# Kernel tuning notes

Hardware: AMD Instinct MI355X
Metric: run time of the kernel (lower is better)

The kernel has to match this reference:

```python
import jax, jax.numpy as jnp
import numpy as np

HIDDEN = 4096
INTER = 11008
B, S = 8, 16
QMAX = 127  # int8 symmetric range for w_bits=8


def setup_inputs() -> dict:
    key = jax.random.key(0)
    ks = jax.random.split(key, 7)
    hidden_state = jax.random.normal(ks[0], (B, S, HIDDEN), dtype=jnp.float32)
    # Quantized weights stored as integer values in float32 (as the dequant source)
    w1_q = jax.random.randint(ks[1], (INTER, HIDDEN), -QMAX - 1, QMAX + 1).astype(jnp.float32)
    w3_q = jax.random.randint(ks[2], (INTER, HIDDEN), -QMAX - 1, QMAX + 1).astype(jnp.float32)
    w2_q = jax.random.randint(ks[3], (HIDDEN, INTER), -QMAX - 1, QMAX + 1).astype(jnp.float32)
    # Per-output-channel dequant scales (has_scale=True)
    w1_s = jax.random.uniform(ks[4], (INTER,), dtype=jnp.float32, minval=0.5, maxval=1.5) * 0.01
    w3_s = jax.random.uniform(ks[5], (INTER,), dtype=jnp.float32, minval=0.5, maxval=1.5) * 0.01
    w2_s = jax.random.uniform(ks[6], (HIDDEN,), dtype=jnp.float32, minval=0.5, maxval=1.5) * 0.01
    return {"hidden_state": hidden_state, "w1_q": w1_q, "w1_s": w1_s,
            "w3_q": w3_q, "w3_s": w3_s, "w2_q": w2_q, "w2_s": w2_s}


def _dequant_linear(x, w_q, w_s):
    # w_q: [out, in] integer-valued weights; w_s: [out] per-channel scale
    # y = x @ (w_q * w_s[:, None]).T == (x @ w_q.T) * w_s
    return jnp.einsum('bsh,oh->bso', x, w_q) * w_s


def reference(hidden_state, w1_q, w1_s, w3_q, w3_s, w2_q, w2_s):
    up = _dequant_linear(hidden_state, w1_q, w1_s)      # [B,S,INTER]
    gate = _dequant_linear(hidden_state, w3_q, w3_s)    # [B,S,INTER]
    h = jax.nn.silu(up) * gate                          # SwiGLU
    return _dequant_linear(h, w2_q, w2_s)               # [B,S,HIDDEN]
```

## Files before the change

kernel.cpp:

```cpp
#include <hip/hip_runtime.h>

#define HIDDEN 4096
#define INTER  11008
#define MTOK   128
#define NMERG  (2*INTER)
#define KS1    4
#define KS2    16

typedef short          short8  __attribute__((ext_vector_type(8)));
typedef unsigned short ushort8 __attribute__((ext_vector_type(8)));
typedef float          f32x16  __attribute__((ext_vector_type(16)));
#define AS1 __attribute__((address_space(1)))
#define AS3 __attribute__((address_space(3)))

static __device__ __forceinline__ unsigned short f2bf_rne(float f) {
    unsigned u = __builtin_bit_cast(unsigned, f);
    u += 0x7FFFu + ((u >> 16) & 1u);
    return (unsigned short)(u >> 16);
}
static __device__ __forceinline__ float bf2f(unsigned short b) {
    unsigned u = (unsigned)b << 16;
    return __builtin_bit_cast(float, u);
}
static __device__ __forceinline__ int pk2(float lo, float hi) {
    return (int)__builtin_amdgcn_perm(__builtin_bit_cast(unsigned, hi),
                                      __builtin_bit_cast(unsigned, lo),
                                      0x07060302u);
}

__global__ void cvt_x_k(const float* __restrict__ x, unsigned short* __restrict__ A2) {
    int f = blockIdx.x * 256 + threadIdx.x;
    int lane = f & 63, w = f >> 6;
    int kstep = w >> 2, ms = w & 3;
    int m = ms * 32 + (lane & 31);
    int k = kstep * 16 + (lane >> 5) * 8;
    const float* src = x + (size_t)m * HIDDEN + k;
    float4 v0 = *(const float4*)(src);
    float4 v1 = *(const float4*)(src + 4);
    ushort8 o;
    o[0] = f2bf_rne(v0.x); o[1] = f2bf_rne(v0.y); o[2] = f2bf_rne(v0.z); o[3] = f2bf_rne(v0.w);
    o[4] = f2bf_rne(v1.x); o[5] = f2bf_rne(v1.y); o[6] = f2bf_rne(v1.z); o[7] = f2bf_rne(v1.w);
    *(ushort8*)(A2 + (size_t)f * 8) = o;
}

template<bool OBF16>
__global__ __launch_bounds__(256) void gemm_k(
    const unsigned short* __restrict__ A2,
    const float* __restrict__ B0, const float* __restrict__ B1, int nhalf,
    void* __restrict__ part, int K, int N, int totTiles, int ksplit)
{
    __shared__ __align__(16) float lds[8192];
    const int lane = threadIdx.x & 63;
    const int ws   = threadIdx.x >> 6;
    const int n0   = blockIdx.x * 128;
    const int ks   = blockIdx.y;
    const int tbeg = (ks * totTiles) / ksplit;
    const int tend = ((ks + 1) * totTiles) / ksplit;

    const char* gbase[8];
#pragma unroll
    for (int i = 0; i < 8; ++i) {
        int s = ws * 512 + i * 64 + lane;
        int n = s >> 4;
        int a = (s & 15) ^ (n & 15);
        const float* rowp = (n0 + n < nhalf) ? (B0 + (size_t)(n0 + n) * K)
                                             : (B1 + (size_t)(n0 + n - nhalf) * K);
        gbase[i] = (const char*)rowp + a * 16;
    }

    f32x16 acc[4];
#pragma unroll
    for (int t = 0; t < 4; ++t)
#pragma unroll
        for (int r = 0; r < 16; ++r) acc[t][r] = 0.f;

    const int nl = ws * 32 + (lane & 31);

    for (int t = tbeg; t < tend; ++t) {
        const size_t koff = (size_t)t * 64 * 4;
#pragma unroll
        for (int i = 0; i < 8; ++i) {
            __builtin_amdgcn_global_load_lds(
                (const AS1 unsigned*)(gbase[i] + koff),
                (AS3 unsigned*)((char*)lds + ws * 8192 + i * 1024), 16, 0, 0);
        }
        __syncthreads();

#pragma unroll
        for (int step = 0; step < 4; ++step) {
            int a0 = step * 4 + ((lane >> 5) << 1);
            int p0 = nl * 16 + (a0 ^ (nl & 15));
            int p1 = nl * 16 + ((a0 + 1) ^ (nl & 15));
            float4 v0 = *(const float4*)((const char*)lds + p0 * 16);
            float4 v1 = *(const float4*)((const char*)lds + p1 * 16);
            int4 bi;
            bi.x = pk2(v0.x, v0.y); bi.y = pk2(v0.z, v0.w);
            bi.z = pk2(v1.x, v1.y); bi.w = pk2(v1.z, v1.w);
            short8 bf = __builtin_bit_cast(short8, bi);
            int kg = t * 4 + step;
#pragma unroll
            for (int ms = 0; ms < 4; ++ms) {
                short8 af = *(const short8*)(A2 + ((size_t)(kg * 4 + ms) * 64 + lane) * 8);
                acc[ms] = __builtin_amdgcn_mfma_f32_32x32x16_bf16(af, bf, acc[ms], 0, 0, 0);
            }
        }
        __syncthreads();
    }

    const int n = n0 + ws * 32 + (lane & 31);
#pragma unroll
    for (int ms = 0; ms < 4; ++ms)
#pragma unroll
        for (int r = 0; r < 16; ++r) {
            int m = ms * 32 + (r & 3) + 8 * (r >> 2) + 4 * (lane >> 5);
            size_t idx = ((size_t)ks * MTOK + m) * (size_t)N + n;
            if (OBF16) ((unsigned short*)part)[idx] = f2bf_rne(acc[ms][r]);
            else       ((float*)part)[idx] = acc[ms][r];
        }
}

__global__ void swiglu_k(const unsigned short* __restrict__ p1,
                         const float* __restrict__ s1, const float* __restrict__ s3,
                         unsigned short* __restrict__ h2)
{
    int f = blockIdx.x * 256 + threadIdx.x;
    int lane = f & 63, w = f >> 6;
    int kstep = w >> 2, ms = w & 3;
    int m = ms * 32 + (lane & 31);
    int j = kstep * 16 + (lane >> 5) * 8;
    float up[8], gt[8];
#pragma unroll
    for (int e = 0; e < 8; ++e) { up[e] = 0.f; gt[e] = 0.f; }
#pragma unroll
    for (int ks = 0; ks < KS1; ++ks) {
        const unsigned short* pu = p1 + ((size_t)ks * MTOK + m) * NMERG + j;
        ushort8 u = *(const ushort8*)(pu);
        ushort8 g = *(const ushort8*)(pu + INTER);
#pragma unroll
        for (int e = 0; e < 8; ++e) { up[e] += bf2f(u[e]); gt[e] += bf2f(g[e]); }
    }
    float4 c1a = *(const float4*)(s1 + j), c1b = *(const float4*)(s1 + j + 4);
    float4 c3a = *(const float4*)(s3 + j), c3b = *(const float4*)(s3 + j + 4);
    float c1[8] = {c1a.x, c1a.y, c1a.z, c1a.w, c1b.x, c1b.y, c1b.z, c1b.w};
    float c3[8] = {c3a.x, c3a.y, c3a.z, c3a.w, c3b.x, c3b.y, c3b.z, c3b.w};
    ushort8 o;
#pragma unroll
    for (int e = 0; e < 8; ++e) {
        float u = up[e] * c1[e], g = gt[e] * c3[e];
        o[e] = f2bf_rne(g * u / (1.f + __expf(-u)));
    }
    *(ushort8*)(h2 + (size_t)f * 8) = o;
}

__global__ void reduce_k(const float* __restrict__ p, const float* __restrict__ s2,
                         float* __restrict__ out)
{
    int i = (blockIdx.x * 256 + threadIdx.x) * 4;
    float4 acc = *(const float4*)(p + i);
#pragma unroll
    for (int s = 1; s < KS2; ++s) {
        float4 v = *(const float4*)(p + (size_t)s * MTOK * HIDDEN + i);
        acc.x += v.x; acc.y += v.y; acc.z += v.z; acc.w += v.w;
    }
    int ncol = i & (HIDDEN - 1);
    float4 sc = *(const float4*)(s2 + ncol);
    acc.x *= sc.x; acc.y *= sc.y; acc.z *= sc.z; acc.w *= sc.w;
    *(float4*)(out + i) = acc;
}

extern "C" void kernel_launch(void* const* d_in, const int* in_sizes, int n_in,
                              void* d_out, int out_size, void* d_ws, size_t ws_size,
                              hipStream_t stream) {
    const float* x   = (const float*)d_in[0];
    const float* w1q = (const float*)d_in[1];
    const float* w1s = (const float*)d_in[2];
    const float* w3q = (const float*)d_in[3];
    const float* w3s = (const float*)d_in[4];
    const float* w2q = (const float*)d_in[5];
    const float* w2s = (const float*)d_in[6];
    float* out = (float*)d_out;

    char* ws = (char*)d_ws;
    unsigned short* xb2 = (unsigned short*)ws;
    unsigned short* h2  = (unsigned short*)(ws + (1u << 20));
    void* part          = (void*)(ws + (4u << 20));

    cvt_x_k<<<MTOK * HIDDEN / 8 / 256, 256, 0, stream>>>(x, xb2);
    gemm_k<true><<<dim3(NMERG / 128, KS1), 256, 0, stream>>>(
        xb2, w1q, w3q, INTER, part, HIDDEN, NMERG, HIDDEN / 64, KS1);
    swiglu_k<<<MTOK * INTER / 8 / 256, 256, 0, stream>>>(
        (const unsigned short*)part, w1s, w3s, h2);
    gemm_k<false><<<dim3(HIDDEN / 128, KS2), 256, 0, stream>>>(
        h2, w2q, w2q, 1 << 30, part, INTER, HIDDEN, INTER / 64, KS2);
    reduce_k<<<MTOK * HIDDEN / 4 / 256, 256, 0, stream>>>(
        (const float*)part, w2s, out);
}
```

Before: 540.6 us.

## Restructure GEMM into independent per-wave 32-column tiles with larger K chunks

The GEMM kernel now gives each wave its own 32-column output tile and its own 32KB LDS buffer, with 128-thread blocks. Each wave streams a 256-wide K chunk per iteration using wave-level s_waitcnt instead of block-wide __syncthreads. The LDS swizzle becomes a lane-rotation scheme, and the second GEMM's split-K drops from 16 to 8, which also shrinks the partial-sum reduction. The aims are to remove block barriers and to put more weight bytes in flight per wave. The cost is 64KB of LDS per block, which limits occupancy, and no double buffering, so load latency is only hidden across waves.

Measured after the change: 781.4 us. +44.5%, slower.

```diff
diff --git a/kernel.cpp b/kernel.cpp
--- a/kernel.cpp
+++ b/kernel.cpp
@@ -5,7 +5,8 @@
 #define MTOK   128
 #define NMERG  (2*INTER)
 #define KS1    4
-#define KS2    16
+#define KS2    8
+#define BKF    256
 
 typedef short          short8  __attribute__((ext_vector_type(8)));
 typedef unsigned short ushort8 __attribute__((ext_vector_type(8)));
@@ -44,29 +45,25 @@
 }
 
 template<bool OBF16>
-__global__ __launch_bounds__(256) void gemm_k(
+__global__ __launch_bounds__(128) void gemm_k(
     const unsigned short* __restrict__ A2,
     const float* __restrict__ B0, const float* __restrict__ B1, int nhalf,
-    void* __restrict__ part, int K, int N, int totTiles, int ksplit)
+    void* __restrict__ part, int K, int N, int ntiles, int nChunksTot, int ksplit)
 {
-    __shared__ __align__(16) float lds[8192];
+    __shared__ __align__(16) char lds[2][32 * 1024];
     const int lane = threadIdx.x & 63;
-    const int ws   = threadIdx.x >> 6;
-    const int n0   = blockIdx.x * 128;
-    const int ks   = blockIdx.y;
-    const int tbeg = (ks * totTiles) / ksplit;
-    const int tend = ((ks + 1) * totTiles) / ksplit;
+    const int wsl  = threadIdx.x >> 6;
+    const int wid  = blockIdx.x * 2 + wsl;
+    const int ntile = wid % ntiles;
+    const int ks    = wid / ntiles;
+    const int n0    = ntile * 32;
+    const int cbeg  = (ks * nChunksTot) / ksplit;
+    const int cend  = ((ks + 1) * nChunksTot) / ksplit;
+    char* buf = lds[wsl];
 
-    const char* gbase[8];
-#pragma unroll
-    for (int i = 0; i < 8; ++i) {
-        int s = ws * 512 + i * 64 + lane;
-        int n = s >> 4;
-        int a = (s & 15) ^ (n & 15);
-        const float* rowp = (n0 + n < nhalf) ? (B0 + (size_t)(n0 + n) * K)
-                                             : (B1 + (size_t)(n0 + n - nhalf) * K);
-        gbase[i] = (const char*)rowp + a * 16;
-    }
+    const float* bbase = (n0 < nhalf) ? (B0 + (size_t)n0 * K)
+                                      : (B1 + (size_t)(n0 - nhalf) * K);
+    const size_t rowbytes = (size_t)K * 4;
 
     f32x16 acc[4];
 #pragma unroll
@@ -74,48 +71,50 @@
 #pragma unroll
         for (int r = 0; r < 16; ++r) acc[t][r] = 0.f;
 
-    const int nl = ws * 32 + (lane & 31);
+    const int r     = lane & 31;
+    const int khalf = lane >> 5;
 
-    for (int t = tbeg; t < tend; ++t) {
-        const size_t koff = (size_t)t * 64 * 4;
+    for (int c = cbeg; c < cend; ++c) {
+        __builtin_amdgcn_s_waitcnt(0xC07F);
+        const char* cb = (const char*)bbase + (size_t)c * (BKF * 4);
 #pragma unroll
-        for (int i = 0; i < 8; ++i) {
+        for (int i = 0; i < 32; ++i) {
+            int soff = ((lane + i) & 63) * 16;
             __builtin_amdgcn_global_load_lds(
-                (const AS1 unsigned*)(gbase[i] + koff),
-                (AS3 unsigned*)((char*)lds + ws * 8192 + i * 1024), 16, 0, 0);
+                (const AS1 unsigned*)(cb + (size_t)i * rowbytes + soff),
+                (AS3 unsigned*)(buf + i * 1024), 16, 0, 0);
         }
-        __syncthreads();
+        __builtin_amdgcn_s_waitcnt(0x0F70);
 
 #pragma unroll
-        for (int step = 0; step < 4; ++step) {
-            int a0 = step * 4 + ((lane >> 5) << 1);
-            int p0 = nl * 16 + (a0 ^ (nl & 15));
-            int p1 = nl * 16 + ((a0 + 1) ^ (nl & 15));
-            float4 v0 = *(const float4*)((const char*)lds + p0 * 16);
-            float4 v1 = *(const float4*)((const char*)lds + p1 * 16);
+        for (int t = 0; t < 16; ++t) {
+            int a0 = t * 4 + khalf * 2;
+            int s0 = (a0 - r) & 63;
+            int s1 = (a0 + 1 - r) & 63;
+            float4 v0 = *(const float4*)(buf + r * 1024 + s0 * 16);
+            float4 v1 = *(const float4*)(buf + r * 1024 + s1 * 16);
             int4 bi;
             bi.x = pk2(v0.x, v0.y); bi.y = pk2(v0.z, v0.w);
             bi.z = pk2(v1.x, v1.y); bi.w = pk2(v1.z, v1.w);
             short8 bf = __builtin_bit_cast(short8, bi);
-            int kg = t * 4 + step;
+            int kg = c * 16 + t;
 #pragma unroll
             for (int ms = 0; ms < 4; ++ms) {
                 short8 af = *(const short8*)(A2 + ((size_t)(kg * 4 + ms) * 64 + lane) * 8);
                 acc[ms] = __builtin_amdgcn_mfma_f32_32x32x16_bf16(af, bf, acc[ms], 0, 0, 0);
             }
         }
-        __syncthreads();
     }
 
-    const int n = n0 + ws * 32 + (lane & 31);
+    const int n = n0 + r;
 #pragma unroll
     for (int ms = 0; ms < 4; ++ms)
 #pragma unroll
-        for (int r = 0; r < 16; ++r) {
-            int m = ms * 32 + (r & 3) + 8 * (r >> 2) + 4 * (lane >> 5);
+        for (int rr = 0; rr < 16; ++rr) {
+            int m = ms * 32 + (rr & 3) + 8 * (rr >> 2) + 4 * khalf;
             size_t idx = ((size_t)ks * MTOK + m) * (size_t)N + n;
-            if (OBF16) ((unsigned short*)part)[idx] = f2bf_rne(acc[ms][r]);
-            else       ((float*)part)[idx] = acc[ms][r];
+            if (OBF16) ((unsigned short*)part)[idx] = f2bf_rne(acc[ms][rr]);
+            else       ((float*)part)[idx] = acc[ms][rr];
         }
 }
 
@@ -186,12 +185,12 @@
     void* part          = (void*)(ws + (4u << 20));
 
     cvt_x_k<<<MTOK * HIDDEN / 8 / 256, 256, 0, stream>>>(x, xb2);
-    gemm_k<true><<<dim3(NMERG / 128, KS1), 256, 0, stream>>>(
-        xb2, w1q, w3q, INTER, part, HIDDEN, NMERG, HIDDEN / 64, KS1);
+    gemm_k<true><<<688 * KS1 / 2, 128, 0, stream>>>(
+        xb2, w1q, w3q, INTER, part, HIDDEN, NMERG, NMERG / 32, HIDDEN / BKF, KS1);
     swiglu_k<<<MTOK * INTER / 8 / 256, 256, 0, stream>>>(
         (const unsigned short*)part, w1s, w3s, h2);
-    gemm_k<false><<<dim3(HIDDEN / 128, KS2), 256, 0, stream>>>(
-        h2, w2q, w2q, 1 << 30, part, INTER, HIDDEN, INTER / 64, KS2);
+    gemm_k<false><<<128 * KS2 / 2, 128, 0, stream>>>(
+        h2, w2q, w2q, 1 << 30, part, INTER, HIDDEN, HIDDEN / 32, INTER / BKF, KS2);
     reduce_k<<<MTOK * HIDDEN / 4 / 256, 256, 0, stream>>>(
         (const float*)part, w2s, out);
 }
```

## Restructure GEMMs to 32-column tiles with fixed 512-K split and in-block K reduction

Applied to the files above, without the earlier changes.

Replaces the looping 128-column GEMM with a single-shot kernel where each 512-thread block loads a 32×512 fp32 weight slab into LDS once. Eight waves split the work over M tiles and two K halves, and the halves are reduced through LDS. The split-K factors rise to 8 and 22, with a separate launch handling the 256-wide K tail of the second GEMM. Partial sums of the down projection are now stored as bf16, which halves partial-buffer traffic but adds rounding error. The aim is more parallel blocks and more memory-level parallelism for streaming the weights, at the cost of more partial writes and an extra launch.

Measured after the change: 570.9 us. 5.6% more time.

```diff
diff --git a/kernel.cpp b/kernel.cpp
--- a/kernel.cpp
+++ b/kernel.cpp
@@ -4,14 +4,12 @@
 #define INTER  11008
 #define MTOK   128
 #define NMERG  (2*INTER)
-#define KS1    4
-#define KS2    16
+#define KS1    8
+#define KS2    22
 
 typedef short          short8  __attribute__((ext_vector_type(8)));
 typedef unsigned short ushort8 __attribute__((ext_vector_type(8)));
 typedef float          f32x16  __attribute__((ext_vector_type(16)));
-#define AS1 __attribute__((address_space(1)))
-#define AS3 __attribute__((address_space(3)))
 
 static __device__ __forceinline__ unsigned short f2bf_rne(float f) {
     unsigned u = __builtin_bit_cast(unsigned, f);
@@ -43,80 +41,83 @@
     *(ushort8*)(A2 + (size_t)f * 8) = o;
 }
 
-template<bool OBF16>
-__global__ __launch_bounds__(256) void gemm_k(
+template<int NKG>
+__global__ __launch_bounds__(512) void gemm_k(
     const unsigned short* __restrict__ A2,
     const float* __restrict__ B0, const float* __restrict__ B1, int nhalf,
-    void* __restrict__ part, int K, int N, int totTiles, int ksplit)
+    unsigned short* __restrict__ part, int K, int N, int ksbase)
 {
-    __shared__ __align__(16) float lds[8192];
-    const int lane = threadIdx.x & 63;
-    const int ws   = threadIdx.x >> 6;
-    const int n0   = blockIdx.x * 128;
-    const int ks   = blockIdx.y;
-    const int tbeg = (ks * totTiles) / ksplit;
-    const int tend = ((ks + 1) * totTiles) / ksplit;
+    __shared__ __align__(16) char lds[65536];
+    const int t    = threadIdx.x;
+    const int lane = t & 63;
+    const int w    = t >> 6;
+    const int n0   = blockIdx.x * 32;
+    const int ksf  = ksbase + blockIdx.y;
+    const int kbeg = ksf * 512;
+    const int rowb = NKG * 64;
+    const int lpr  = NKG / 16;
 
-    const char* gbase[8];
+    const float* bb = ((n0 < nhalf) ? (B0 + (size_t)n0 * K)
+                                    : (B1 + (size_t)(n0 - nhalf) * K)) + kbeg;
 #pragma unroll
-    for (int i = 0; i < 8; ++i) {
-        int s = ws * 512 + i * 64 + lane;
-        int n = s >> 4;
-        int a = (s & 15) ^ (n & 15);
-        const float* rowp = (n0 + n < nhalf) ? (B0 + (size_t)(n0 + n) * K)
-                                             : (B1 + (size_t)(n0 + n - nhalf) * K);
-        gbase[i] = (const char*)rowp + a * 16;
+    for (int j = 0; j < 4 * lpr; ++j) {
+        int r    = 4 * w + ((lpr == 2) ? (j >> 1) : j);
+        int half = (lpr == 2) ? (j & 1) : 0;
+        int atom = half * 64 + lane;
+        float4 v = *(const float4*)((const char*)bb + (size_t)r * (K * 4)
+                                    + half * 1024 + lane * 16);
+        *(float4*)(lds + r * rowb + ((atom ^ (r & 7)) * 16)) = v;
     }
+    __syncthreads();
 
-    f32x16 acc[4];
+    const int ms = w >> 1, h = w & 1;
+    const int half = NKG / 2;
+    const int r  = lane & 31;
+    const int kh = lane >> 5;
+    f32x16 acc;
 #pragma unroll
-    for (int t = 0; t < 4; ++t)
-#pragma unroll
-        for (int r = 0; r < 16; ++r) acc[t][r] = 0.f;
-
-    const int nl = ws * 32 + (lane & 31);
-
-    for (int t = tbeg; t < tend; ++t) {
-        const size_t koff = (size_t)t * 64 * 4;
-#pragma unroll
-        for (int i = 0; i < 8; ++i) {
-            __builtin_amdgcn_global_load_lds(
-                (const AS1 unsigned*)(gbase[i] + koff),
-                (AS3 unsigned*)((char*)lds + ws * 8192 + i * 1024), 16, 0, 0);
-        }
-        __syncthreads();
+    for (int i = 0; i < 16; ++i) acc[i] = 0.f;
 
 #pragma unroll
-        for (int step = 0; step < 4; ++step) {
-            int a0 = step * 4 + ((lane >> 5) << 1);
-            int p0 = nl * 16 + (a0 ^ (nl & 15));
-            int p1 = nl * 16 + ((a0 + 1) ^ (nl & 15));
-            float4 v0 = *(const float4*)((const char*)lds + p0 * 16);
-            float4 v1 = *(const float4*)((const char*)lds + p1 * 16);
-            int4 bi;
-            bi.x = pk2(v0.x, v0.y); bi.y = pk2(v0.z, v0.w);
-            bi.z = pk2(v1.x, v1.y); bi.w = pk2(v1.z, v1.w);
-            short8 bf = __builtin_bit_cast(short8, bi);
-            int kg = t * 4 + step;
+    for (int kg = h * half; kg < h * half + half; ++kg) {
+        int a0 = kg * 4 + kh * 2;
+        float4 v0 = *(const float4*)(lds + r * rowb + ((a0 ^ (r & 7)) * 16));
+        float4 v1 = *(const float4*)(lds + r * rowb + (((a0 + 1) ^ (r & 7)) * 16));
+        int4 bi;
+        bi.x = pk2(v0.x, v0.y); bi.y = pk2(v0.z, v0.w);
+        bi.z = pk2(v1.x, v1.y); bi.w = pk2(v1.z, v1.w);
+        short8 bf = __builtin_bit_cast(short8, bi);
+        int kstep = (kbeg >> 4) + kg;
+        short8 af = *(const short8*)(A2 + ((size_t)(kstep * 4 + ms) * 64 + lane) * 8);
+        acc = __builtin_amdgcn_mfma_f32_32x32x16_bf16(af, bf, acc, 0, 0, 0);
+    }
+    __syncthreads();
+
+    {
+        char* rb = lds + (size_t)(w * 64 + lane) * 72;
 #pragma unroll
-            for (int ms = 0; ms < 4; ++ms) {
-                short8 af = *(const short8*)(A2 + ((size_t)(kg * 4 + ms) * 64 + lane) * 8);
-                acc[ms] = __builtin_amdgcn_mfma_f32_32x32x16_bf16(af, bf, acc[ms], 0, 0, 0);
-            }
+        for (int q = 0; q < 4; ++q)
+            *(float4*)(rb + q * 16) = *(const float4*)((const float*)&acc + q * 4);
+    }
+    __syncthreads();
+
+    const int msp = t >> 7;
+    const int lp  = (t >> 1) & 63;
+    const int qp  = t & 1;
+    const int n   = n0 + (lp & 31);
+    const int khp = lp >> 5;
+#pragma unroll
+    for (int qq = 0; qq < 2; ++qq) {
+        int q = qp * 2 + qq;
+        float4 s0 = *(const float4*)(lds + (size_t)(((msp * 2 + 0) * 64 + lp)) * 72 + q * 16);
+        float4 s1 = *(const float4*)(lds + (size_t)(((msp * 2 + 1) * 64 + lp)) * 72 + q * 16);
+        float s[4] = {s0.x + s1.x, s0.y + s1.y, s0.z + s1.z, s0.w + s1.w};
+#pragma unroll
+        for (int e = 0; e < 4; ++e) {
+            int m = msp * 32 + e + 8 * q + 4 * khp;
+            part[((size_t)ksf * MTOK + m) * (size_t)N + n] = f2bf_rne(s[e]);
         }
-        __syncthreads();
     }
-
-    const int n = n0 + ws * 32 + (lane & 31);
-#pragma unroll
-    for (int ms = 0; ms < 4; ++ms)
-#pragma unroll
-        for (int r = 0; r < 16; ++r) {
-            int m = ms * 32 + (r & 3) + 8 * (r >> 2) + 4 * (lane >> 5);
-            size_t idx = ((size_t)ks * MTOK + m) * (size_t)N + n;
-            if (OBF16) ((unsigned short*)part)[idx] = f2bf_rne(acc[ms][r]);
-            else       ((float*)part)[idx] = acc[ms][r];
-        }
 }
 
 __global__ void swiglu_k(const unsigned short* __restrict__ p1,
@@ -152,20 +153,20 @@
     *(ushort8*)(h2 + (size_t)f * 8) = o;
 }
 
-__global__ void reduce_k(const float* __restrict__ p, const float* __restrict__ s2,
+__global__ void reduce_k(const unsigned short* __restrict__ p, const float* __restrict__ s2,
                          float* __restrict__ out)
 {
     int i = (blockIdx.x * 256 + threadIdx.x) * 4;
-    float4 acc = *(const float4*)(p + i);
+    float a[4] = {0.f, 0.f, 0.f, 0.f};
 #pragma unroll
-    for (int s = 1; s < KS2; ++s) {
-        float4 v = *(const float4*)(p + (size_t)s * MTOK * HIDDEN + i);
-        acc.x += v.x; acc.y += v.y; acc.z += v.z; acc.w += v.w;
+    for (int s = 0; s < KS2; ++s) {
+        ushort4 v = *(const ushort4*)(p + (size_t)s * MTOK * HIDDEN + i);
+        a[0] += bf2f(v.x); a[1] += bf2f(v.y); a[2] += bf2f(v.z); a[3] += bf2f(v.w);
     }
     int ncol = i & (HIDDEN - 1);
     float4 sc = *(const float4*)(s2 + ncol);
-    acc.x *= sc.x; acc.y *= sc.y; acc.z *= sc.z; acc.w *= sc.w;
-    *(float4*)(out + i) = acc;
+    float4 o = {a[0] * sc.x, a[1] * sc.y, a[2] * sc.z, a[3] * sc.w};
+    *(float4*)(out + i) = o;
 }
 
 extern "C" void kernel_launch(void* const* d_in, const int* in_sizes, int n_in,
@@ -183,15 +184,15 @@
     char* ws = (char*)d_ws;
     unsigned short* xb2 = (unsigned short*)ws;
     unsigned short* h2  = (unsigned short*)(ws + (1u << 20));
-    void* part          = (void*)(ws + (4u << 20));
+    unsigned short* part = (unsigned short*)(ws + (4u << 20));
 
     cvt_x_k<<<MTOK * HIDDEN / 8 / 256, 256, 0, stream>>>(x, xb2);
-    gemm_k<true><<<dim3(NMERG / 128, KS1), 256, 0, stream>>>(
-        xb2, w1q, w3q, INTER, part, HIDDEN, NMERG, HIDDEN / 64, KS1);
-    swiglu_k<<<MTOK * INTER / 8 / 256, 256, 0, stream>>>(
-        (const unsigned short*)part, w1s, w3s, h2);
-    gemm_k<false><<<dim3(HIDDEN / 128, KS2), 256, 0, stream>>>(
-        h2, w2q, w2q, 1 << 30, part, INTER, HIDDEN, INTER / 64, KS2);
-    reduce_k<<<MTOK * HIDDEN / 4 / 256, 256, 0, stream>>>(
-        (const float*)part, w2s, out);
+    gemm_k<32><<<dim3(NMERG / 32, KS1), 512, 0, stream>>>(
+        xb2, w1q, w3q, INTER, part, HIDDEN, NMERG, 0);
+    swiglu_k<<<MTOK * INTER / 8 / 256, 256, 0, stream>>>(part, w1s, w3s, h2);
+    gemm_k<32><<<dim3(HIDDEN / 32, KS2 - 1), 512, 0, stream>>>(
+        h2, w2q, w2q, 1 << 30, part, INTER, HIDDEN, 0);
+    gemm_k<16><<<dim3(HIDDEN / 32, 1), 512, 0, stream>>>(
+        h2, w2q, w2q, 1 << 30, part, INTER, HIDDEN, KS2 - 1);
+    reduce_k<<<MTOK * HIDDEN / 4 / 256, 256, 0, stream>>>(part, w2s, out);
 }
```
